# Kernel tuning notes

Hardware: AMD Instinct MI355X
Metric: run time of the kernel (lower is better)

## Reference

```python
import jax, jax.numpy as jnp
import numpy as np

B, S, D, H, E, K = 8, 4096, 512, 2048, 8, 2


def setup_inputs() -> dict:
    key = jax.random.key(0)
    ks = jax.random.split(key, 8)
    def lin(k, shape, fan_in):
        return jax.random.normal(k, shape, jnp.float32) / np.sqrt(fan_in).astype(np.float32)
    return {
        "x": jax.random.normal(ks[0], (B, S, D), jnp.float32),
        "noise": jax.random.normal(ks[1], (B, S, E), jnp.float32),
        "Wg": lin(ks[2], (D, E), D), "bg": jnp.zeros((E,), jnp.float32),
        "Wn": lin(ks[3], (D, E), D), "bn": jnp.zeros((E,), jnp.float32),
        "W1": lin(ks[4], (E, D, H), D), "b1": jnp.zeros((E, H), jnp.float32),
        "W2": lin(ks[5], (E, H, D), H), "b2": jnp.zeros((E, D), jnp.float32),
    }


def reference(x, noise, Wg, bg, Wn, bn, W1, b1, W2, b2):
    # Noisy top-k router
    logits = x @ Wg + bg                                  # [B,S,E]
    noise_logits = x @ Wn + bn                            # [B,S,E]
    noisy = logits + noise * jax.nn.softplus(noise_logits)
    _, topi = jax.lax.top_k(noisy, K)                     # [B,S,K]
    # sparse softmax: -inf everywhere except the top-k expert slots
    sel = (topi[..., :, None] == jnp.arange(E)).any(axis=-2)  # [B,S,E] bool
    sparse = jnp.where(sel, noisy, -jnp.inf)
    gates = jax.nn.softmax(sparse, axis=-1)               # [B,S,E]; zeros off top-k
    # Combine: gates are exactly 0 for unselected experts, so the masked
    # gather-MLP-scatter loop equals a gate-weighted sum of expert MLPs.
    # (Expert dropout is identity in eval mode.)
    out = jnp.zeros_like(x)
    for e in range(E):  # small fixed expert count
        h = jax.nn.relu(x @ W1[e] + b1[e])                # [B,S,H]
        y = h @ W2[e] + b2[e]                             # [B,S,D]
        out = out + y * gates[..., e:e + 1]
    return out
```

## Files before the change

### kernel.cpp

```cpp
#include <hip/hip_runtime.h>

#define TT 32768
#define DD 512
#define HH 2048
#define EE 8
#define CAP 8192

typedef unsigned short u16;
typedef unsigned int u32;
typedef unsigned long long u64;
using short8  = __attribute__((ext_vector_type(8))) short;
using floatx4 = __attribute__((ext_vector_type(4))) float;

__device__ __forceinline__ u16 f2bf(float f) {
  unsigned u = __float_as_uint(f);
  u += 0x7FFFu + ((u >> 16) & 1u);
  return (u16)(u >> 16);
}

__device__ __forceinline__ void gl2lds16(const u16* g, char* l) {
  __builtin_amdgcn_global_load_lds(
      (const __attribute__((address_space(1))) u32*)(const void*)g,
      (__attribute__((address_space(3))) u32*)(void*)l, 16, 0, 0);
}

__global__ void transpose_bf16(const float* __restrict__ in, u16* __restrict__ out, int R, int C) {
  __shared__ float tile[32][33];
  int e = blockIdx.z;
  const float* src = in + (size_t)e * R * C;
  u16* dst = out + (size_t)e * R * C;
  int tx = threadIdx.x, ty = threadIdx.y;
  int c0 = blockIdx.x * 32, r0 = blockIdx.y * 32;
#pragma unroll
  for (int i = 0; i < 32; i += 8)
    tile[ty + i][tx] = src[(size_t)(r0 + ty + i) * C + c0 + tx];
  __syncthreads();
#pragma unroll
  for (int i = 0; i < 32; i += 8)
    dst[(size_t)(c0 + ty + i) * R + r0 + tx] = f2bf(tile[tx][ty + i]);
}

__global__ void prep_router_w(const float* __restrict__ Wg, const float* __restrict__ Wn,
                              float* __restrict__ wrt) {
  int c = blockIdx.x;
  int k = threadIdx.x;
  wrt[c * 512 + k] = (c < 8) ? Wg[k * 8 + c] : Wn[k * 8 + (c - 8)];
}

__global__ __launch_bounds__(256)
void router_topk(const float* __restrict__ x, const float* __restrict__ noise,
                 const float* __restrict__ wrt, const float* __restrict__ bg,
                 const float* __restrict__ bn,
                 u16* __restrict__ xb, int* __restrict__ topk_i,
                 float* __restrict__ tg0, float* __restrict__ tg1) {
  __shared__ __align__(16) float xs[16 * 516];
  __shared__ __align__(16) float wls[16 * 516];
  const int tid = threadIdx.x;
  const int blk = blockIdx.x;
  {
    const float4* wg4 = (const float4*)wrt;
#pragma unroll
    for (int j = 0; j < 8; ++j) {
      int L = tid + j * 256;
      int c = L >> 7, c4 = L & 127;
      *(float4*)(wls + c * 516 + c4 * 4) = wg4[L];
    }
  }
  const float4* xg = (const float4*)(x + (size_t)blk * 16 * DD);
  ushort4* xo = (ushort4*)(xb + (size_t)blk * 16 * DD);
#pragma unroll
  for (int j = 0; j < 8; ++j) {
    int L = tid + j * 256;
    int tk = L >> 7, j4 = L & 127;
    float4 v = xg[L];
    *(float4*)(xs + tk * 516 + j4 * 4) = v;
    ushort4 o; o.x = f2bf(v.x); o.y = f2bf(v.y); o.z = f2bf(v.z); o.w = f2bf(v.w);
    xo[L] = o;
  }
  __syncthreads();
  const int tok = tid >> 4;
  const int col = tid & 15;
  const float4* xr = (const float4*)(xs + tok * 516);
  const float4* wr = (const float4*)(wls + col * 516);
  float acc = 0.f;
#pragma unroll 8
  for (int k = 0; k < 128; ++k) {
    float4 xv = xr[k];
    float4 wv = wr[k];
    acc += xv.x * wv.x + xv.y * wv.y + xv.z * wv.z + xv.w * wv.w;
  }
  const int t = blk * 16 + tok;
  float other = __shfl_xor(acc, 8);
  float noisy = -3.4e38f;
  if (col < 8) {
    float nl = other + bn[col];
    float sp = (nl > 20.f) ? nl : log1pf(expf(nl));
    noisy = acc + bg[col] + noise[(size_t)t * EE + col] * sp;
  }
  float v = noisy; int vi = col;
#pragma unroll
  for (int off = 1; off <= 4; off <<= 1) {
    float ov = __shfl_xor(v, off);
    int   oi = __shfl_xor(vi, off);
    if (ov > v || (ov == v && oi < vi)) { v = ov; vi = oi; }
  }
  float v2 = (col == vi) ? -3.4e38f : noisy;
  int vi2 = col;
#pragma unroll
  for (int off = 1; off <= 4; off <<= 1) {
    float ov = __shfl_xor(v2, off);
    int   oi = __shfl_xor(vi2, off);
    if (ov > v2 || (ov == v2 && oi < vi2)) { v2 = ov; vi2 = oi; }
  }
  if (col == 0) {
    float ed = expf(v2 - v);
    float inv = 1.f / (1.f + ed);
    topk_i[t] = vi | (vi2 << 8);
    tg0[t] = inv;
    tg1[t] = ed * inv;
  }
}

__global__ void router_bin(const int* __restrict__ topk_i, const float* __restrict__ tg0,
                           const float* __restrict__ tg1,
                           int* __restrict__ countsA, int* __restrict__ countsB,
                           int* __restrict__ listsA, int* __restrict__ listsB,
                           float* __restrict__ gatesA, float* __restrict__ gatesB) {
  __shared__ int histA[EE], histB[EE], baseA[EE], baseB[EE];
  int t = blockIdx.x * 256 + threadIdx.x;
  if (threadIdx.x < EE) { histA[threadIdx.x] = 0; histB[threadIdx.x] = 0; }
  __syncthreads();
  int p = topk_i[t];
  int i0 = p & 255, i1 = p >> 8;
  int r0 = atomicAdd(&histA[i0], 1);
  int r1 = atomicAdd(&histB[i1], 1);
  __syncthreads();
  if (threadIdx.x < EE) {
    baseA[threadIdx.x] = atomicAdd(&countsA[threadIdx.x], histA[threadIdx.x]);
    baseB[threadIdx.x] = atomicAdd(&countsB[threadIdx.x], histB[threadIdx.x]);
  }
  __syncthreads();
  int s0 = baseA[i0] + r0, s1 = baseB[i1] + r1;
  if (s0 < CAP) { listsA[i0 * CAP + s0] = t; gatesA[i0 * CAP + s0] = tg0[t]; }
  if (s1 < CAP) { listsB[i1 * CAP + s1] = t; gatesB[i1 * CAP + s1] = tg1[t]; }
}

#define MS1 8
#define MS2 32
__global__ __launch_bounds__(256, 2)
void pass1_gemm(const u16* __restrict__ xb, const u16* __restrict__ w1t,
                const float* __restrict__ b1, const int* __restrict__ counts,
                const int* __restrict__ lists, u16* __restrict__ H) {
  __shared__ __align__(16) char lds[32768];
  char* ldsA = lds;
  char* ldsB = lds + 16384;
  const int e = blockIdx.x & 7;
  const int nt = (blockIdx.x >> 3) & 15;
  const int ms = blockIdx.x >> 7;
  int cnt = counts[e]; if (cnt > CAP) cnt = CAP;
  int eOff = 0;
#pragma unroll
  for (int j = 0; j < EE; ++j) {
    int cj = counts[j]; if (cj > CAP) cj = CAP;
    eOff += (j < e) ? cj : 0;
  }
  const int tid = threadIdx.x, lane = tid & 63, w = tid >> 6;
  const int col16 = lane & 15, quad = lane >> 4;
  const int hh = w & 1, mh = w >> 1;

  int rowi[4], kqi[4];
  const u16* wptr[4];
#pragma unroll
  for (int i = 0; i < 4; ++i) {
    int c = tid + i * 256;
    rowi[i] = c >> 3;
    kqi[i] = (c & 7) ^ (rowi[i] & 7);
    wptr[i] = w1t + (size_t)(e * HH + nt * 128 + rowi[i]) * DD + kqi[i] * 8;
  }

  for (int mtile = ms; mtile * 128 < cnt; mtile += MS1) {
    const u16* xptr[4];
#pragma unroll
    for (int i = 0; i < 4; ++i) {
      int idx = mtile * 128 + rowi[i];
      int tok = (idx < cnt) ? lists[e * CAP + idx] : 0;
      xptr[i] = xb + (size_t)tok * DD + kqi[i] * 8;
    }
    floatx4 acc[4][4];
#pragma unroll
    for (int a = 0; a < 4; ++a)
#pragma unroll
      for (int b = 0; b < 4; ++b) acc[a][b] = (floatx4){0.f, 0.f, 0.f, 0.f};

    for (int kc = 0; kc < DD / 64; ++kc) {
      __syncthreads();
#pragma unroll
      for (int i = 0; i < 4; ++i) {
        int off = (tid + i * 256) * 16;
        gl2lds16(wptr[i] + kc * 64, ldsA + off);
        gl2lds16(xptr[i] + kc * 64, ldsB + off);
      }
      __syncthreads();
#pragma unroll
      for (int ks = 0; ks < 2; ++ks) {
        short8 af[4], bf[4];
#pragma unroll
        for (int t4 = 0; t4 < 4; ++t4) {
          int rA = hh * 64 + t4 * 16 + col16;
          af[t4] = *(const short8*)(ldsA + (rA * 8 + ((ks * 4 + quad) ^ (rA & 7))) * 16);
          int rB = mh * 64 + t4 * 16 + col16;
          bf[t4] = *(const short8*)(ldsB + (rB * 8 + ((ks * 4 + quad) ^ (rB & 7))) * 16);
        }
#pragma unroll
        for (int ht = 0; ht < 4; ++ht)
#pragma unroll
          for (int mt = 0; mt < 4; ++mt)
            acc[ht][mt] = __builtin_amdgcn_mfma_f32_16x16x32_bf16(af[ht], bf[mt], acc[ht][mt], 0, 0, 0);
      }
    }
#pragma unroll
    for (int ht = 0; ht < 4; ++ht) {
      int hloc = nt * 128 + hh * 64 + ht * 16 + quad * 4;
      float b1v[4];
#pragma unroll
      for (int r = 0; r < 4; ++r) b1v[r] = b1[e * HH + hloc + r];
#pragma unroll
      for (int mt = 0; mt < 4; ++mt) {
        int gm = mtile * 128 + mh * 64 + mt * 16 + col16;
        if (gm < cnt) {
          u64 pk = 0;
#pragma unroll
          for (int r = 0; r < 4; ++r) {
            float f = fmaxf(acc[ht][mt][r] + b1v[r], 0.f);
            pk |= (u64)f2bf(f) << (16 * r);
          }
          *(u64*)(H + (size_t)(eOff + gm) * HH + hloc) = pk;
        }
      }
    }
  }
}

__global__ __launch_bounds__(256, 2)
void pass2_gemm(const u16* __restrict__ H, const u16* __restrict__ w2t,
                const float* __restrict__ b2, const int* __restrict__ counts,
                const int* __restrict__ lists, const float* __restrict__ gates,
                float* __restrict__ out, int rmw) {
  __shared__ __align__(16) char lds[32768];
  char* ldsA = lds;
  char* ldsB = lds + 16384;
  const int e = blockIdx.x & 7;
  const int nt = (blockIdx.x >> 3) & 3;
  const int ms = blockIdx.x >> 5;
  int cnt = counts[e]; if (cnt > CAP) cnt = CAP;
  int eOff = 0;
#pragma unroll
  for (int j = 0; j < EE; ++j) {
    int cj = counts[j]; if (cj > CAP) cj = CAP;
    eOff += (j < e) ? cj : 0;
  }
  const int tid = threadIdx.x, lane = tid & 63, w = tid >> 6;
  const int col16 = lane & 15, quad = lane >> 4;
  const int mh = w & 1, dh = w >> 1;

  int rowi[4], kqi[4];
  const u16* wptr[4];
#pragma unroll
  for (int i = 0; i < 4; ++i) {
    int c = tid + i * 256;
    rowi[i] = c >> 3;
    kqi[i] = (c & 7) ^ (rowi[i] & 7);
    wptr[i] = w2t + (size_t)(e * DD + nt * 128 + rowi[i]) * HH + kqi[i] * 8;
  }

  for (int mtile = ms; mtile * 128 < cnt; mtile += MS2) {
    const u16* hptr[4];
#pragma unroll
    for (int i = 0; i < 4; ++i)
      hptr[i] = H + (size_t)(eOff + mtile * 128 + rowi[i]) * HH + kqi[i] * 8;

    floatx4 acc[4][4];
#pragma unroll
    for (int a = 0; a < 4; ++a)
#pragma unroll
      for (int b = 0; b < 4; ++b) acc[a][b] = (floatx4){0.f, 0.f, 0.f, 0.f};

    for (int kc = 0; kc < HH / 64; ++kc) {
      __syncthreads();
#pragma unroll
      for (int i = 0; i < 4; ++i) {
        int off = (tid + i * 256) * 16;
        gl2lds16(hptr[i] + kc * 64, ldsA + off);
        gl2lds16(wptr[i] + kc * 64, ldsB + off);
      }
      __syncthreads();
#pragma unroll
      for (int ks = 0; ks < 2; ++ks) {
        short8 af[4], bf[4];
#pragma unroll
        for (int t4 = 0; t4 < 4; ++t4) {
          int rA = mh * 64 + t4 * 16 + col16;
          af[t4] = *(const short8*)(ldsA + (rA * 8 + ((ks * 4 + quad) ^ (rA & 7))) * 16);
          int rB = dh * 64 + t4 * 16 + col16;
          bf[t4] = *(const short8*)(ldsB + (rB * 8 + ((ks * 4 + quad) ^ (rB & 7))) * 16);
        }
#pragma unroll
        for (int mt = 0; mt < 4; ++mt)
#pragma unroll
          for (int dt = 0; dt < 4; ++dt)
            acc[mt][dt] = __builtin_amdgcn_mfma_f32_16x16x32_bf16(af[mt], bf[dt], acc[mt][dt], 0, 0, 0);
      }
    }
    float b2v[4];
#pragma unroll
    for (int dt = 0; dt < 4; ++dt)
      b2v[dt] = b2[e * DD + nt * 128 + dh * 64 + dt * 16 + col16];
#pragma unroll
    for (int mt = 0; mt < 4; ++mt) {
#pragma unroll
      for (int r = 0; r < 4; ++r) {
        int idx = mtile * 128 + mh * 64 + mt * 16 + quad * 4 + r;
        if (idx < cnt) {
          int tok = lists[e * CAP + idx];
          float g = gates[e * CAP + idx];
          float* orow = out + (size_t)tok * DD + nt * 128 + dh * 64;
          if (rmw) {
#pragma unroll
            for (int dt = 0; dt < 4; ++dt)
              orow[dt * 16 + col16] += g * (acc[mt][dt][r] + b2v[dt]);
          } else {
#pragma unroll
            for (int dt = 0; dt < 4; ++dt)
              orow[dt * 16 + col16] = g * (acc[mt][dt][r] + b2v[dt]);
          }
        }
      }
    }
  }
}

extern "C" void kernel_launch(void* const* d_in, const int* in_sizes, int n_in,
                              void* d_out, int out_size, void* d_ws, size_t ws_size,
                              hipStream_t stream) {
  const float* x     = (const float*)d_in[0];
  const float* noise = (const float*)d_in[1];
  const float* Wg    = (const float*)d_in[2];
  const float* bg    = (const float*)d_in[3];
  const float* Wn    = (const float*)d_in[4];
  const float* bn    = (const float*)d_in[5];
  const float* W1    = (const float*)d_in[6];
  const float* b1    = (const float*)d_in[7];
  const float* W2    = (const float*)d_in[8];
  const float* b2    = (const float*)d_in[9];
  float* out = (float*)d_out;
  char* ws = (char*)d_ws;

  u16*  w1t     = (u16*)(ws + 0x0000000);
  u16*  w2t     = (u16*)(ws + 0x1000000);
  u16*  xb      = (u16*)(ws + 0x2000000);
  int*  countsA = (int*)(ws + 0x4000000);
  int*  countsB = (int*)(ws + 0x4000020);
  float* wrt    = (float*)(ws + 0x4002000);
  int*  listsA  = (int*)(ws + 0x4010000);
  int*  listsB  = (int*)(ws + 0x4050000);
  float* gatesA = (float*)(ws + 0x4090000);
  float* gatesB = (float*)(ws + 0x40D0000);
  int*  topk_i  = (int*)(ws + 0x4110000);
  float* tg0    = (float*)(ws + 0x4130000);
  float* tg1    = (float*)(ws + 0x4150000);
  u16*  Hbuf    = (u16*)(ws + 0x4170000);
  (void)ws_size;

  hipMemsetAsync(countsA, 0, 64, stream);
  prep_router_w<<<16, 512, 0, stream>>>(Wg, Wn, wrt);
  transpose_bf16<<<dim3(HH / 32, DD / 32, EE), dim3(32, 8), 0, stream>>>(W1, w1t, DD, HH);
  transpose_bf16<<<dim3(DD / 32, HH / 32, EE), dim3(32, 8), 0, stream>>>(W2, w2t, HH, DD);
  router_topk<<<TT / 16, 256, 0, stream>>>(x, noise, wrt, bg, bn, xb, topk_i, tg0, tg1);
  router_bin<<<TT / 256, 256, 0, stream>>>(topk_i, tg0, tg1, countsA, countsB,
                                           listsA, listsB, gatesA, gatesB);

  pass1_gemm<<<8 * 16 * MS1, 256, 0, stream>>>(xb, w1t, b1, countsA, listsA, Hbuf);
  pass2_gemm<<<8 * 4 * MS2, 256, 0, stream>>>(Hbuf, w2t, b2, countsA, listsA, gatesA, out, 0);
  pass1_gemm<<<8 * 16 * MS1, 256, 0, stream>>>(xb, w1t, b1, countsB, listsB, Hbuf);
  pass2_gemm<<<8 * 4 * MS2, 256, 0, stream>>>(Hbuf, w2t, b2, countsB, listsB, gatesB, out, 1);
}
```

Before: 662.1 us.

## Double-buffer LDS tiles in both expert GEMM passes to overlap loads with MFMA

Both grouped GEMM kernels now use two 32 KB LDS stages. The next K-chunk is prefetched with global_load_lds while MFMAs run on the current chunk, which replaces the two barriers per K step with one. This is meant to hide global-memory latency behind compute. In exchange, LDS per block grows to 64 KB, which could limit how many blocks fit on a CU alongside the requested two.

```diff
diff --git a/kernel.cpp b/kernel.cpp
--- a/kernel.cpp
+++ b/kernel.cpp
@@ -151,9 +151,7 @@
 void pass1_gemm(const u16* __restrict__ xb, const u16* __restrict__ w1t,
                 const float* __restrict__ b1, const int* __restrict__ counts,
                 const int* __restrict__ lists, u16* __restrict__ H) {
-  __shared__ __align__(16) char lds[32768];
-  char* ldsA = lds;
-  char* ldsB = lds + 16384;
+  __shared__ __align__(16) char lds[65536];
   const int e = blockIdx.x & 7;
   const int nt = (blockIdx.x >> 3) & 15;
   const int ms = blockIdx.x >> 7;
@@ -192,15 +190,26 @@
 #pragma unroll
       for (int b = 0; b < 4; ++b) acc[a][b] = (floatx4){0.f, 0.f, 0.f, 0.f};
 
+#pragma unroll
+    for (int i = 0; i < 4; ++i) {
+      int off = (tid + i * 256) * 16;
+      gl2lds16(wptr[i], lds + off);
+      gl2lds16(xptr[i], lds + 16384 + off);
+    }
+    __syncthreads();
+    int cur = 0;
     for (int kc = 0; kc < DD / 64; ++kc) {
-      __syncthreads();
-#pragma unroll
-      for (int i = 0; i < 4; ++i) {
-        int off = (tid + i * 256) * 16;
-        gl2lds16(wptr[i] + kc * 64, ldsA + off);
-        gl2lds16(xptr[i] + kc * 64, ldsB + off);
-      }
-      __syncthreads();
+      if (kc < DD / 64 - 1) {
+        char* nb = lds + (cur ^ 1) * 32768;
+#pragma unroll
+        for (int i = 0; i < 4; ++i) {
+          int off = (tid + i * 256) * 16;
+          gl2lds16(wptr[i] + (kc + 1) * 64, nb + off);
+          gl2lds16(xptr[i] + (kc + 1) * 64, nb + 16384 + off);
+        }
+      }
+      char* ldsA = lds + cur * 32768;
+      char* ldsB = ldsA + 16384;
 #pragma unroll
       for (int ks = 0; ks < 2; ++ks) {
         short8 af[4], bf[4];
@@ -217,6 +226,8 @@
           for (int mt = 0; mt < 4; ++mt)
             acc[ht][mt] = __builtin_amdgcn_mfma_f32_16x16x32_bf16(af[ht], bf[mt], acc[ht][mt], 0, 0, 0);
       }
+      __syncthreads();
+      cur ^= 1;
     }
 #pragma unroll
     for (int ht = 0; ht < 4; ++ht) {
@@ -246,9 +257,7 @@
                 const float* __restrict__ b2, const int* __restrict__ counts,
                 const int* __restrict__ lists, const float* __restrict__ gates,
                 float* __restrict__ out, int rmw) {
-  __shared__ __align__(16) char lds[32768];
-  char* ldsA = lds;
-  char* ldsB = lds + 16384;
+  __shared__ __align__(16) char lds[65536];
   const int e = blockIdx.x & 7;
   const int nt = (blockIdx.x >> 3) & 3;
   const int ms = blockIdx.x >> 5;
@@ -285,15 +294,26 @@
 #pragma unroll
       for (int b = 0; b < 4; ++b) acc[a][b] = (floatx4){0.f, 0.f, 0.f, 0.f};
 
+#pragma unroll
+    for (int i = 0; i < 4; ++i) {
+      int off = (tid + i * 256) * 16;
+      gl2lds16(hptr[i], lds + off);
+      gl2lds16(wptr[i], lds + 16384 + off);
+    }
+    __syncthreads();
+    int cur = 0;
     for (int kc = 0; kc < HH / 64; ++kc) {
-      __syncthreads();
-#pragma unroll
-      for (int i = 0; i < 4; ++i) {
-        int off = (tid + i * 256) * 16;
-        gl2lds16(hptr[i] + kc * 64, ldsA + off);
-        gl2lds16(wptr[i] + kc * 64, ldsB + off);
-      }
-      __syncthreads();
+      if (kc < HH / 64 - 1) {
+        char* nb = lds + (cur ^ 1) * 32768;
+#pragma unroll
+        for (int i = 0; i < 4; ++i) {
+          int off = (tid + i * 256) * 16;
+          gl2lds16(hptr[i] + (kc + 1) * 64, nb + off);
+          gl2lds16(wptr[i] + (kc + 1) * 64, nb + 16384 + off);
+        }
+      }
+      char* ldsA = lds + cur * 32768;
+      char* ldsB = ldsA + 16384;
 #pragma unroll
       for (int ks = 0; ks < 2; ++ks) {
         short8 af[4], bf[4];
@@ -310,6 +330,8 @@
           for (int dt = 0; dt < 4; ++dt)
             acc[mt][dt] = __builtin_amdgcn_mfma_f32_16x16x32_bf16(af[mt], bf[dt], acc[mt][dt], 0, 0, 0);
       }
+      __syncthreads();
+      cur ^= 1;
     }
     float b2v[4];
 #pragma unroll
```

New measurement: 623.1 us. 5.9% less time.
